# Performance work log

Hardware: AMD Instinct MI355X
Metric: run time of the kernel (lower is better)

The kernel has to match this reference:

```python
import jax, jax.numpy as jnp
import numpy as np

N, E, IN, HID, G, OUT = 50000, 800000, 9, 128, 256, 10
CLUSTERS, NCO, MCO = 20, 6, 4  # numerator deg 5 (6 coeffs), denominator deg 4
EPS = 1e-5


def _gcn(x, W, b, src, dst):
    # PyG GCNConv: x' = D^-1/2 (A + I) D^-1/2 (x W) + b, with self-loops
    n = x.shape[0]
    h = x @ W  # [N, out]
    ones = jnp.ones(src.shape[0], h.dtype)
    deg = jax.ops.segment_sum(ones, dst, num_segments=n) + 1.0  # + self-loop
    dinv = jax.lax.rsqrt(deg)
    coef = (dinv[src] * dinv[dst])[:, None]
    agg = jax.ops.segment_sum(h[src] * coef, dst, num_segments=n)
    agg = agg + h * (dinv * dinv)[:, None]  # self-loop messages
    return agg + b


def _rational(x, num, den, assign):
    # per-cluster safe Pade rational: P_5(x) / (1 + |Q_4(x)|), coeffs gathered per channel
    a = num[assign]  # [HID, 6]
    q = den[assign]  # [HID, 4]
    P = a[:, 5]
    for i in (4, 3, 2, 1, 0):
        P = P * x + a[:, i]
    Q = q[:, 3]
    for i in (2, 1, 0):
        Q = Q * x + q[:, i]
    Q = Q * x  # Q has no constant term
    return P / (1.0 + jnp.abs(Q))


def _bn(x, g, b):
    m = x.mean(axis=0)
    v = x.var(axis=0)
    return g * (x - m) * jax.lax.rsqrt(v + EPS) + b


def setup_inputs() -> dict:
    key = jax.random.key(0)
    ks = jax.random.split(key, 32)
    d = {}
    d["x"] = jax.random.normal(ks[0], (N, IN), jnp.float32)
    d["edge_index"] = jax.random.randint(ks[1], (2, E), 0, N, jnp.int32)
    d["batch"] = jnp.sort(jax.random.randint(ks[2], (N,), 0, G, jnp.int32))
    dims = [(IN, HID), (HID, HID), (HID, HID), (HID, HID)]
    for i, (di, do) in enumerate(dims):
        d[f"W{i}"] = jax.random.normal(ks[3 + i], (di, do), jnp.float32) / np.sqrt(di)
        d[f"b{i}"] = jnp.zeros((do,), jnp.float32)
        d[f"g{i}"] = jnp.ones((do,), jnp.float32)
        d[f"be{i}"] = jnp.zeros((do,), jnp.float32)
    d["rat_num"] = jax.random.normal(ks[10], (CLUSTERS, NCO), jnp.float32) * 0.3
    d["rat_den"] = jax.random.normal(ks[11], (CLUSTERS, MCO), jnp.float32) * 0.3
    d["cluster_assign"] = (jnp.arange(HID) % CLUSTERS).astype(jnp.int32)
    d["HW1"] = jax.random.normal(ks[12], (HID, HID), jnp.float32) / np.sqrt(HID)
    d["Hb1"] = jnp.zeros((HID,), jnp.float32)
    d["HW2"] = jax.random.normal(ks[13], (HID, HID), jnp.float32) / np.sqrt(HID)
    d["Hb2"] = jnp.zeros((HID,), jnp.float32)
    d["HW3"] = jax.random.normal(ks[14], (HID, OUT), jnp.float32) / np.sqrt(HID)
    d["Hb3"] = jnp.zeros((OUT,), jnp.float32)
    return d


def reference(x, edge_index, batch,
              W0, b0, g0, be0, W1, b1, g1, be1,
              W2, b2, g2, be2, W3, b3, g3, be3,
              rat_num, rat_den, cluster_assign,
              HW1, Hb1, HW2, Hb2, HW3, Hb3):
    src, dst = edge_index[0], edge_index[1]
    h = x
    for W, b, g, be in ((W0, b0, g0, be0), (W1, b1, g1, be1),
                        (W2, b2, g2, be2), (W3, b3, g3, be3)):
        h = _gcn(h, W, b, src, dst)
        h = _rational(h, rat_num, rat_den, cluster_assign)
        h = _bn(h, g, be)
        # Dropout(p=0.1): identity in eval mode
    # global mean pool over graphs
    counts = jax.ops.segment_sum(jnp.ones((h.shape[0],), h.dtype), batch, num_segments=G)
    pooled = jax.ops.segment_sum(h, batch, num_segments=G) / jnp.maximum(counts, 1.0)[:, None]
    # MLP head: (Dropout->Linear->GELU) x2, Dropout->Linear
    z = jax.nn.gelu(pooled @ HW1 + Hb1, approximate=False)
    z = jax.nn.gelu(z @ HW2 + Hb2, approximate=False)
    return z @ HW3 + Hb3
```

## Files before the change

kernel.cpp:

```cpp
#include <hip/hip_runtime.h>
#include <math.h>

#define HID 128
#define GRP 256
#define INF 9
#define OUTF 10

typedef _Float16 half8 __attribute__((ext_vector_type(8)));
typedef __attribute__((ext_vector_type(4))) float f32x4;

__global__ void hist_prepw_kernel(const int* __restrict__ ei, int* __restrict__ cnt, int E,
                                  const float* __restrict__ W1, const float* __restrict__ W2,
                                  const float* __restrict__ W3,
                                  _Float16* __restrict__ Whi, _Float16* __restrict__ Wlo) {
    int e = blockIdx.x * 256 + threadIdx.x;
    if (e < E) atomicAdd(&cnt[ei[E + e]], 1);
    if (blockIdx.x < 192) {
        int l = blockIdx.x >> 6;
        int idx = (blockIdx.x & 63) * 256 + threadIdx.x;
        const float* W = (l == 0) ? W1 : (l == 1) ? W2 : W3;
        int nn = idx >> 7, k = idx & 127;
        float w = W[k * HID + nn];
        _Float16 hi = (_Float16)w;
        _Float16 lo = (_Float16)(w - (float)hi);
        int nt = nn >> 4, l16 = nn & 15;
        int kc = k >> 5, quad = (k >> 3) & 3, j = k & 7;
        size_t off = (size_t)(l + 1) * HID * HID +
                     ((((nt * 4 + kc) * 4 + quad) * 16 + l16) * 8 + j);
        Whi[off] = hi;
        Wlo[off] = lo;
    }
}

__global__ __launch_bounds__(256) void scanA_kernel(const int* __restrict__ cnt,
                                                    int* __restrict__ bsum, int n) {
    int tid = threadIdx.x;
    int base = blockIdx.x * 1024 + tid * 4;
    int s = 0;
    #pragma unroll
    for (int i = 0; i < 4; i++) s += (base + i < n) ? cnt[base + i] : 0;
    #pragma unroll
    for (int off = 32; off > 0; off >>= 1) s += __shfl_down(s, off);
    __shared__ int ws[4];
    if ((tid & 63) == 0) ws[tid >> 6] = s;
    __syncthreads();
    if (tid == 0) bsum[blockIdx.x] = ws[0] + ws[1] + ws[2] + ws[3];
}

__global__ void scanB_kernel(int* __restrict__ bsum, int* __restrict__ row_ptr,
                             int nb, int n) {
    int lane = threadIdx.x;
    int carry = 0;
    for (int base = 0; base < nb; base += 64) {
        int v = (base + lane < nb) ? bsum[base + lane] : 0;
        int ps = v;
        #pragma unroll
        for (int off = 1; off < 64; off <<= 1) {
            int t = __shfl_up(ps, off);
            if (lane >= off) ps += t;
        }
        if (base + lane < nb) bsum[base + lane] = carry + ps - v;
        carry += __shfl(ps, 63);
    }
    if (lane == 0) row_ptr[n] = carry;
}

__global__ __launch_bounds__(256) void scanC_kernel(const int* __restrict__ cnt,
                                                    const int* __restrict__ bsum,
                                                    const int* __restrict__ batch,
                                                    int* __restrict__ row_ptr,
                                                    int* __restrict__ cursor,
                                                    float* __restrict__ dinv,
                                                    int* __restrict__ gstart,
                                                    int* __restrict__ gend, int n) {
    int tid = threadIdx.x;
    int lane = tid & 63, wid = tid >> 6;
    int idx0 = blockIdx.x * 1024 + tid * 4;
    int v[4];
    #pragma unroll
    for (int i = 0; i < 4; i++) v[i] = (idx0 + i < n) ? cnt[idx0 + i] : 0;
    int s = v[0] + v[1] + v[2] + v[3];
    int ps = s;
    #pragma unroll
    for (int off = 1; off < 64; off <<= 1) {
        int t = __shfl_up(ps, off);
        if (lane >= off) ps += t;
    }
    __shared__ int wsum[4];
    if (lane == 63) wsum[wid] = ps;
    __syncthreads();
    int woff = 0;
    #pragma unroll
    for (int i = 0; i < 4; i++) if (i < wid) woff += wsum[i];
    int run = bsum[blockIdx.x] + woff + (ps - s);
    #pragma unroll
    for (int i = 0; i < 4; i++) {
        int idx = idx0 + i;
        if (idx < n) {
            row_ptr[idx] = run;
            cursor[idx] = run;
            dinv[idx] = rsqrtf((float)(v[i] + 1));
            run += v[i];
            int b = batch[idx];
            if (idx == 0 || batch[idx - 1] != b) gstart[b] = idx;
            if (idx == n - 1 || batch[idx + 1] != b) gend[b] = idx + 1;
        }
    }
}

__global__ void fill_kernel(const int* __restrict__ ei, int* __restrict__ cursor,
                            const float* __restrict__ dinv,
                            int2* __restrict__ csr, int E) {
    int e = blockIdx.x * blockDim.x + threadIdx.x;
    if (e >= E) return;
    int s = ei[e], d = ei[E + e];
    int pos = atomicAdd(&cursor[d], 1);
    csr[pos] = make_int2(s, __float_as_int(dinv[s] * dinv[d]));
}

__device__ __forceinline__ float rational_act(float xv, const float* __restrict__ a,
                                              const float* __restrict__ q) {
    float P = a[5];
    P = fmaf(P, xv, a[4]); P = fmaf(P, xv, a[3]); P = fmaf(P, xv, a[2]);
    P = fmaf(P, xv, a[1]); P = fmaf(P, xv, a[0]);
    float Q = q[3];
    Q = fmaf(Q, xv, q[2]); Q = fmaf(Q, xv, q[1]); Q = fmaf(Q, xv, q[0]);
    Q *= xv;
    return P / (1.0f + fabsf(Q));
}

__global__ __launch_bounds__(256) void aggx_kernel(const float* __restrict__ x,
                                                   const int* __restrict__ row_ptr,
                                                   const int2* __restrict__ csr,
                                                   const float* __restrict__ dinv,
                                                   float* __restrict__ aggX,
                                                   float* __restrict__ cagg, int n) {
    int tid = threadIdx.x;
    int node = blockIdx.x * 16 + (tid >> 4);
    int lane = tid & 15;
    if (node >= n) return;
    float di = dinv[node];
    float self = di * di;
    float acc = (lane < INF) ? x[node * INF + lane] * self : 0.0f;
    float cfs = self;
    int beg = row_ptr[node], end = row_ptr[node + 1];
    for (int j = beg; j < end; j++) {
        int2 p = csr[j];
        float cf = __int_as_float(p.y);
        cfs += cf;
        if (lane < INF) acc = fmaf(cf, x[p.x * INF + lane], acc);
    }
    if (lane < INF) aggX[node * INF + lane] = acc;
    if (lane == 0) cagg[node] = cfs;
}

__global__ __launch_bounds__(256) void gemm0_fused_kernel(const float* __restrict__ aggX,
                                                          const float* __restrict__ W0,
                                                          const float* __restrict__ b0,
                                                          const float* __restrict__ rat_num,
                                                          const float* __restrict__ rat_den,
                                                          const int* __restrict__ cl_assign,
                                                          _Float16* __restrict__ act,
                                                          float* __restrict__ stat, int n) {
    __shared__ float Ws[INF * HID];
    __shared__ float s_num[120], s_den[80];
    __shared__ int s_cl[HID];
    __shared__ float s_b[HID];
    __shared__ float s_sum[HID], s_sq[HID];
    int tid = threadIdx.x;
    for (int i = tid; i < INF * HID; i += 256) Ws[i] = W0[i];
    if (tid < 120) s_num[tid] = rat_num[tid];
    if (tid < 80) s_den[tid] = rat_den[tid];
    if (tid < HID) {
        s_cl[tid] = cl_assign[tid];
        s_b[tid] = b0[tid];
        s_sum[tid] = 0.0f; s_sq[tid] = 0.0f;
    }
    __syncthreads();
    int c = tid & 127;
    int half = tid >> 7;
    const float* a = s_num + s_cl[c] * 6;
    const float* q = s_den + s_cl[c] * 4;
    float psum = 0.0f, psq = 0.0f;
    for (int node = blockIdx.x * 2 + half; node < n; node += gridDim.x * 2) {
        float acc = s_b[c];
        #pragma unroll
        for (int k = 0; k < INF; k++) acc = fmaf(aggX[node * INF + k], Ws[k * HID + c], acc);
        float r = rational_act(acc, a, q);
        act[node * HID + c] = (_Float16)r;
        psum += r; psq = fmaf(r, r, psq);
    }
    atomicAdd(&s_sum[c], psum);
    atomicAdd(&s_sq[c], psq);
    __syncthreads();
    if (tid < HID) {
        atomicAdd(&stat[tid], s_sum[tid]);
        atomicAdd(&stat[HID + tid], s_sq[tid]);
    }
}

__global__ __launch_bounds__(256) void layer_fused_kernel(const _Float16* __restrict__ act,
                                                          const int2* __restrict__ csr,
                                                          const int* __restrict__ row_ptr,
                                                          const float* __restrict__ dinv,
                                                          const float* __restrict__ cagg,
                                                          const float* __restrict__ statPrev,
                                                          const float* __restrict__ gPrev,
                                                          const float* __restrict__ bePrev,
                                                          const _Float16* __restrict__ Whi,
                                                          const _Float16* __restrict__ Wlo,
                                                          const float* __restrict__ bias,
                                                          const float* __restrict__ rat_num,
                                                          const float* __restrict__ rat_den,
                                                          const int* __restrict__ cl_assign,
                                                          _Float16* __restrict__ actOut,
                                                          float* __restrict__ statOut, int n) {
    __shared__ _Float16 Alds[64 * 136];
    __shared__ int2 s_pair[16][16];
    __shared__ float s_bnw[HID], s_bnu[HID];
    __shared__ float s_num[120], s_den[80];
    __shared__ int s_cl[HID];
    __shared__ float s_bias[HID];
    __shared__ float s_sum[HID], s_sq[HID];
    int tid = threadIdx.x;
    if (tid < 120) s_num[tid] = rat_num[tid];
    if (tid < 80) s_den[tid] = rat_den[tid];
    if (tid < HID) {
        float inv_n = 1.0f / (float)n;
        float mean = statPrev[tid] * inv_n;
        float var = statPrev[HID + tid] * inv_n - mean * mean;
        float w = gPrev[tid] * rsqrtf(var + 1e-5f);
        s_bnw[tid] = w;
        s_bnu[tid] = bePrev[tid] - mean * w;
        s_cl[tid] = cl_assign[tid];
        s_bias[tid] = bias[tid];
        s_sum[tid] = 0.0f; s_sq[tid] = 0.0f;
    }
    __syncthreads();

    int r0 = blockIdx.x * 64;
    int grp = tid >> 4, glane = tid & 15;
    const half8* act8 = (const half8*)act;

    for (int sub = 0; sub < 4; sub++) {
        int lrow = sub * 16 + grp;
        int node = r0 + lrow;
        half8 o;
        if (node < n) {
            float di = dinv[node];
            float selfc = di * di;
            half8 sv = act8[node * 16 + glane];
            float acc[8];
            #pragma unroll
            for (int t = 0; t < 8; t++) acc[t] = (float)sv[t] * selfc;
            int beg = row_ptr[node], end = row_ptr[node + 1];
            for (int base = beg; base < end; base += 16) {
                int m = end - base; if (m > 16) m = 16;
                if (glane < m) s_pair[grp][glane] = csr[base + glane];
                __builtin_amdgcn_wave_barrier();
                int j = 0;
                for (; j + 4 <= m; j += 4) {
                    int2 p0 = s_pair[grp][j],     p1 = s_pair[grp][j + 1];
                    int2 p2 = s_pair[grp][j + 2], p3 = s_pair[grp][j + 3];
                    half8 v0 = act8[p0.x * 16 + glane];
                    half8 v1 = act8[p1.x * 16 + glane];
                    half8 v2 = act8[p2.x * 16 + glane];
                    half8 v3 = act8[p3.x * 16 + glane];
                    float c0 = __int_as_float(p0.y), c1 = __int_as_float(p1.y);
                    float c2 = __int_as_float(p2.y), c3 = __int_as_float(p3.y);
                    #pragma unroll
                    for (int t = 0; t < 8; t++) {
                        acc[t] = fmaf(c0, (float)v0[t], acc[t]);
                        acc[t] = fmaf(c1, (float)v1[t], acc[t]);
                        acc[t] = fmaf(c2, (float)v2[t], acc[t]);
                        acc[t] = fmaf(c3, (float)v3[t], acc[t]);
                    }
                }
                for (; j < m; j++) {
                    int2 p = s_pair[grp][j];
                    float cf = __int_as_float(p.y);
                    half8 v = act8[p.x * 16 + glane];
                    #pragma unroll
                    for (int t = 0; t < 8; t++) acc[t] = fmaf(cf, (float)v[t], acc[t]);
                }
                __builtin_amdgcn_wave_barrier();
            }
            float cg = cagg[node];
            #pragma unroll
            for (int t = 0; t < 8; t++) {
                int c = glane * 8 + t;
                o[t] = (_Float16)fmaf(s_bnw[c], acc[t], s_bnu[c] * cg);
            }
        } else {
            #pragma unroll
            for (int t = 0; t < 8; t++) o[t] = (_Float16)0.0f;
        }
        *(half8*)&Alds[lrow * 136 + glane * 8] = o;
    }
    __syncthreads();

    int w = tid >> 6, l64 = tid & 63;
    int quad = l64 >> 4, l16 = l64 & 15;
    const half8* Bh8 = (const half8*)Whi;
    const half8* Bl8 = (const half8*)Wlo;
    f32x4 acc[8];
    #pragma unroll
    for (int j = 0; j < 8; j++) acc[j] = (f32x4){0.f, 0.f, 0.f, 0.f};
    int lrowA = w * 16 + l16;
    #pragma unroll
    for (int kc = 0; kc < 4; kc++) {
        half8 a = *(const half8*)&Alds[lrowA * 136 + kc * 32 + quad * 8];
        #pragma unroll
        for (int nt = 0; nt < 8; nt++) {
            half8 bh = Bh8[(nt * 4 + kc) * 64 + l64];
            half8 bl = Bl8[(nt * 4 + kc) * 64 + l64];
            acc[nt] = __builtin_amdgcn_mfma_f32_16x16x32_f16(a, bh, acc[nt], 0, 0, 0);
            acc[nt] = __builtin_amdgcn_mfma_f32_16x16x32_f16(a, bl, acc[nt], 0, 0, 0);
        }
    }

    float ps[8], pq[8];
    #pragma unroll
    for (int nt = 0; nt < 8; nt++) { ps[nt] = 0.0f; pq[nt] = 0.0f; }
    #pragma unroll
    for (int reg = 0; reg < 4; reg++) {
        int row = r0 + w * 16 + quad * 4 + reg;
        if (row < n) {
            #pragma unroll
            for (int nt = 0; nt < 8; nt++) {
                int col = nt * 16 + l16;
                float v = acc[nt][reg] + s_bias[col];
                float r = rational_act(v, s_num + s_cl[col] * 6, s_den + s_cl[col] * 4);
                actOut[row * HID + col] = (_Float16)r;
                ps[nt] += r; pq[nt] = fmaf(r, r, pq[nt]);
            }
        }
    }
    #pragma unroll
    for (int nt = 0; nt < 8; nt++) {
        int col = nt * 16 + l16;
        atomicAdd(&s_sum[col], ps[nt]);
        atomicAdd(&s_sq[col], pq[nt]);
    }
    __syncthreads();
    if (tid < HID) {
        atomicAdd(&statOut[tid], s_sum[tid]);
        atomicAdd(&statOut[HID + tid], s_sq[tid]);
    }
}

__global__ __launch_bounds__(256) void poolmlp_kernel(const _Float16* __restrict__ act,
                                                      const int* __restrict__ gstart,
                                                      const int* __restrict__ gend,
                                                      const float* __restrict__ stat,
                                                      const float* __restrict__ g3,
                                                      const float* __restrict__ be3,
                                                      const float* __restrict__ HW1,
                                                      const float* __restrict__ Hb1,
                                                      const float* __restrict__ HW2,
                                                      const float* __restrict__ Hb2,
                                                      const float* __restrict__ HW3,
                                                      const float* __restrict__ Hb3,
                                                      float* __restrict__ out, int n) {
    __shared__ float red[16][HID];
    __shared__ float s_pool[HID];
    __shared__ float s_z[HID];
    int gi = blockIdx.x;
    int tid = threadIdx.x;
    int rg = tid >> 4, lane = tid & 15;
    int s = gstart[gi], e = gend[gi];
    const half8* act8 = (const half8*)act;
    float a[8];
    #pragma unroll
    for (int t = 0; t < 8; t++) a[t] = 0.0f;
    for (int r = s + rg; r < e; r += 16) {
        half8 v = act8[r * 16 + lane];
        #pragma unroll
        for (int t = 0; t < 8; t++) a[t] += (float)v[t];
    }
    #pragma unroll
    for (int t = 0; t < 8; t++) red[rg][lane * 8 + t] = a[t];
    __syncthreads();
    if (tid < HID) {
        float tot = 0.0f;
        #pragma unroll
        for (int i = 0; i < 16; i++) tot += red[i][tid];
        int cnt = e - s;
        float pooled = 0.0f;
        if (cnt > 0) {
            float inv_n = 1.0f / (float)n;
            float mean = stat[tid] * inv_n;
            float var = stat[HID + tid] * inv_n - mean * mean;
            float w = g3[tid] * rsqrtf(var + 1e-5f);
            float u = be3[tid] - mean * w;
            pooled = fmaf(w, tot / (float)cnt, u);
        }
        s_pool[tid] = pooled;
    }
    __syncthreads();
    if (tid < HID) {
        float acc = Hb1[tid];
        #pragma unroll 8
        for (int k = 0; k < HID; k++) acc = fmaf(s_pool[k], HW1[k * HID + tid], acc);
        s_z[tid] = 0.5f * acc * (1.0f + erff(acc * 0.70710678118654752f));
    }
    __syncthreads();
    if (tid < HID) {
        float acc = Hb2[tid];
        #pragma unroll 8
        for (int k = 0; k < HID; k++) acc = fmaf(s_z[k], HW2[k * HID + tid], acc);
        s_pool[tid] = 0.5f * acc * (1.0f + erff(acc * 0.70710678118654752f));
    }
    __syncthreads();
    if (tid < OUTF) {
        float acc = Hb3[tid];
        #pragma unroll 8
        for (int k = 0; k < HID; k++) acc = fmaf(s_pool[k], HW3[k * OUTF + tid], acc);
        out[gi * OUTF + tid] = acc;
    }
}

extern "C" void kernel_launch(void* const* d_in, const int* in_sizes, int n_in,
                              void* d_out, int out_size, void* d_ws, size_t ws_size,
                              hipStream_t stream) {
    const float* x          = (const float*)d_in[0];
    const int*   edge_index = (const int*)d_in[1];
    const int*   batch      = (const int*)d_in[2];
    const float* W[4]  = {(const float*)d_in[3], (const float*)d_in[7], (const float*)d_in[11], (const float*)d_in[15]};
    const float* bL[4] = {(const float*)d_in[4], (const float*)d_in[8], (const float*)d_in[12], (const float*)d_in[16]};
    const float* gL[4] = {(const float*)d_in[5], (const float*)d_in[9], (const float*)d_in[13], (const float*)d_in[17]};
    const float* beL[4]= {(const float*)d_in[6], (const float*)d_in[10], (const float*)d_in[14], (const float*)d_in[18]};
    const float* rat_num = (const float*)d_in[19];
    const float* rat_den = (const float*)d_in[20];
    const int*   cl_assign = (const int*)d_in[21];
    const float* HW1 = (const float*)d_in[22];
    const float* Hb1 = (const float*)d_in[23];
    const float* HW2 = (const float*)d_in[24];
    const float* Hb2 = (const float*)d_in[25];
    const float* HW3 = (const float*)d_in[26];
    const float* Hb3 = (const float*)d_in[27];
    float* out = (float*)d_out;

    const int N = in_sizes[0] / INF;
    const int E = in_sizes[1] / 2;
    const int NB = (N + 1023) / 1024;

    char* wsb = (char*)d_ws;
    size_t o = 0;
    #define ALIGN16 o = (o + 3) & ~(size_t)3;
    int*   cnt     = (int*)(wsb + o * 4);  o += N; ALIGN16
    int*   gstart  = (int*)(wsb + o * 4);  o += GRP;
    int*   gend    = (int*)(wsb + o * 4);  o += GRP;
    float* bnstat  = (float*)(wsb + o * 4); o += 4 * 256;
    size_t zero_elems = o;
    int*   bsum    = (int*)(wsb + o * 4);  o += ((NB + 63) & ~63); ALIGN16
    int*   cursor  = (int*)(wsb + o * 4);  o += N; ALIGN16
    int*   row_ptr = (int*)(wsb + o * 4);  o += N + 1; ALIGN16
    float* dinv    = (float*)(wsb + o * 4); o += N; ALIGN16
    int2*  csr     = (int2*)(wsb + o * 4);  o += 2 * (size_t)E; ALIGN16
    float* aggX    = (float*)(wsb + o * 4); o += (size_t)N * INF; ALIGN16
    _Float16* WhiAll = (_Float16*)(wsb + o * 4); o += 4 * HID * HID / 2; ALIGN16
    _Float16* WloAll = (_Float16*)(wsb + o * 4); o += 4 * HID * HID / 2; ALIGN16
    _Float16* act_h  = (_Float16*)(wsb + o * 4); o += (size_t)N * HID / 2;
    float* cagg = (float*)cnt;

    hipMemsetAsync(d_ws, 0, zero_elems * 4, stream);

    int eb = (E + 255) / 256;
    hist_prepw_kernel<<<eb, 256, 0, stream>>>(edge_index, cnt, E, W[1], W[2], W[3],
                                              WhiAll, WloAll);
    scanA_kernel<<<NB, 256, 0, stream>>>(cnt, bsum, N);
    scanB_kernel<<<1, 64, 0, stream>>>(bsum, row_ptr, NB, N);
    scanC_kernel<<<NB, 256, 0, stream>>>(cnt, bsum, batch, row_ptr, cursor, dinv,
                                         gstart, gend, N);
    fill_kernel<<<eb, 256, 0, stream>>>(edge_index, cursor, dinv, csr, E);

    aggx_kernel<<<(N + 15) / 16, 256, 0, stream>>>(x, row_ptr, csr, dinv, aggX, cagg, N);
    gemm0_fused_kernel<<<1024, 256, 0, stream>>>(aggX, W[0], bL[0], rat_num, rat_den,
                                                 cl_assign, act_h, bnstat, N);

    int layer_grid = (N + 63) / 64;
    for (int l = 1; l < 4; l++) {
        layer_fused_kernel<<<layer_grid, 256, 0, stream>>>(act_h, csr, row_ptr, dinv, cagg,
                                                           bnstat + (l - 1) * 256,
                                                           gL[l - 1], beL[l - 1],
                                                           WhiAll + (size_t)l * HID * HID,
                                                           WloAll + (size_t)l * HID * HID,
                                                           bL[l], rat_num, rat_den, cl_assign,
                                                           act_h, bnstat + l * 256, N);
    }
    poolmlp_kernel<<<GRP, 256, 0, stream>>>(act_h, gstart, gend, bnstat + 3 * 256,
                                            gL[3], beL[3], HW1, Hb1, HW2, Hb2, HW3, Hb3,
                                            out, N);
}
```

Before: 516.1 us.

## Use 512-thread 32-row blocks with wave-split MFMA and ping-pong activations

The fused GCN layer kernel now launches 512-thread blocks covering 32 nodes. Each 16-lane group aggregates a single node instead of looping over four, and the 128x128 MFMA GEMM is split across 8 waves as 2 row tiles by 4 column pairs. This is meant to expose more parallelism for the latency-bound neighbour gather and to cut per-thread accumulator registers. Activations also move from one buffer updated in place to two alternating buffers. That removes a read-after-write race between blocks gathering neighbour rows, at the cost of an extra N×128 half buffer.

```diff
diff --git a/kernel.cpp b/kernel.cpp
--- a/kernel.cpp
+++ b/kernel.cpp
@@ -199,7 +199,7 @@
     }
 }
 
-__global__ __launch_bounds__(256) void layer_fused_kernel(const _Float16* __restrict__ act,
+__global__ __launch_bounds__(512, 8) void layer_fused_kernel(const _Float16* __restrict__ act,
                                                           const int2* __restrict__ csr,
                                                           const int* __restrict__ row_ptr,
                                                           const float* __restrict__ dinv,
@@ -215,8 +215,8 @@
                                                           const int* __restrict__ cl_assign,
                                                           _Float16* __restrict__ actOut,
                                                           float* __restrict__ statOut, int n) {
-    __shared__ _Float16 Alds[64 * 136];
-    __shared__ int2 s_pair[16][16];
+    __shared__ _Float16 Alds[32 * 136];
+    __shared__ int2 s_pair[32][16];
     __shared__ float s_bnw[HID], s_bnu[HID];
     __shared__ float s_num[120], s_den[80];
     __shared__ int s_cl[HID];
@@ -238,13 +238,12 @@
     }
     __syncthreads();
 
-    int r0 = blockIdx.x * 64;
+    int r0 = blockIdx.x * 32;
     int grp = tid >> 4, glane = tid & 15;
     const half8* act8 = (const half8*)act;
 
-    for (int sub = 0; sub < 4; sub++) {
-        int lrow = sub * 16 + grp;
-        int node = r0 + lrow;
+    {
+        int node = r0 + grp;
         half8 o;
         if (node < n) {
             float di = dinv[node];
@@ -295,53 +294,53 @@
             #pragma unroll
             for (int t = 0; t < 8; t++) o[t] = (_Float16)0.0f;
         }
-        *(half8*)&Alds[lrow * 136 + glane * 8] = o;
+        *(half8*)&Alds[grp * 136 + glane * 8] = o;
     }
     __syncthreads();
 
     int w = tid >> 6, l64 = tid & 63;
     int quad = l64 >> 4, l16 = l64 & 15;
+    int mtile = w & 1, npair = w >> 1;
     const half8* Bh8 = (const half8*)Whi;
     const half8* Bl8 = (const half8*)Wlo;
-    f32x4 acc[8];
-    #pragma unroll
-    for (int j = 0; j < 8; j++) acc[j] = (f32x4){0.f, 0.f, 0.f, 0.f};
-    int lrowA = w * 16 + l16;
+    f32x4 acc0 = (f32x4){0.f, 0.f, 0.f, 0.f};
+    f32x4 acc1 = (f32x4){0.f, 0.f, 0.f, 0.f};
+    int lrowA = mtile * 16 + l16;
     #pragma unroll
     for (int kc = 0; kc < 4; kc++) {
         half8 a = *(const half8*)&Alds[lrowA * 136 + kc * 32 + quad * 8];
-        #pragma unroll
-        for (int nt = 0; nt < 8; nt++) {
-            half8 bh = Bh8[(nt * 4 + kc) * 64 + l64];
-            half8 bl = Bl8[(nt * 4 + kc) * 64 + l64];
-            acc[nt] = __builtin_amdgcn_mfma_f32_16x16x32_f16(a, bh, acc[nt], 0, 0, 0);
-            acc[nt] = __builtin_amdgcn_mfma_f32_16x16x32_f16(a, bl, acc[nt], 0, 0, 0);
+        int nt0 = npair * 2, nt1 = npair * 2 + 1;
+        half8 bh0 = Bh8[(nt0 * 4 + kc) * 64 + l64];
+        half8 bl0 = Bl8[(nt0 * 4 + kc) * 64 + l64];
+        half8 bh1 = Bh8[(nt1 * 4 + kc) * 64 + l64];
+        half8 bl1 = Bl8[(nt1 * 4 + kc) * 64 + l64];
+        acc0 = __builtin_amdgcn_mfma_f32_16x16x32_f16(a, bh0, acc0, 0, 0, 0);
+        acc0 = __builtin_amdgcn_mfma_f32_16x16x32_f16(a, bl0, acc0, 0, 0, 0);
+        acc1 = __builtin_amdgcn_mfma_f32_16x16x32_f16(a, bh1, acc1, 0, 0, 0);
+        acc1 = __builtin_amdgcn_mfma_f32_16x16x32_f16(a, bl1, acc1, 0, 0, 0);
+    }
+
+    float ps0 = 0.f, pq0 = 0.f, ps1 = 0.f, pq1 = 0.f;
+    int col0 = (npair * 2) * 16 + l16;
+    int col1 = (npair * 2 + 1) * 16 + l16;
+    #pragma unroll
+    for (int reg = 0; reg < 4; reg++) {
+        int row = r0 + mtile * 16 + quad * 4 + reg;
+        if (row < n) {
+            float v0 = acc0[reg] + s_bias[col0];
+            float r0v = rational_act(v0, s_num + s_cl[col0] * 6, s_den + s_cl[col0] * 4);
+            actOut[row * HID + col0] = (_Float16)r0v;
+            ps0 += r0v; pq0 = fmaf(r0v, r0v, pq0);
+            float v1 = acc1[reg] + s_bias[col1];
+            float r1v = rational_act(v1, s_num + s_cl[col1] * 6, s_den + s_cl[col1] * 4);
+            actOut[row * HID + col1] = (_Float16)r1v;
+            ps1 += r1v; pq1 = fmaf(r1v, r1v, pq1);
         }
     }
-
-    float ps[8], pq[8];
-    #pragma unroll
-    for (int nt = 0; nt < 8; nt++) { ps[nt] = 0.0f; pq[nt] = 0.0f; }
-    #pragma unroll
-    for (int reg = 0; reg < 4; reg++) {
-        int row = r0 + w * 16 + quad * 4 + reg;
-        if (row < n) {
-            #pragma unroll
-            for (int nt = 0; nt < 8; nt++) {
-                int col = nt * 16 + l16;
-                float v = acc[nt][reg] + s_bias[col];
-                float r = rational_act(v, s_num + s_cl[col] * 6, s_den + s_cl[col] * 4);
-                actOut[row * HID + col] = (_Float16)r;
-                ps[nt] += r; pq[nt] = fmaf(r, r, pq[nt]);
-            }
-        }
-    }
-    #pragma unroll
-    for (int nt = 0; nt < 8; nt++) {
-        int col = nt * 16 + l16;
-        atomicAdd(&s_sum[col], ps[nt]);
-        atomicAdd(&s_sq[col], pq[nt]);
-    }
+    atomicAdd(&s_sum[col0], ps0);
+    atomicAdd(&s_sq[col0], pq0);
+    atomicAdd(&s_sum[col1], ps1);
+    atomicAdd(&s_sq[col1], pq1);
     __syncthreads();
     if (tid < HID) {
         atomicAdd(&statOut[tid], s_sum[tid]);
@@ -461,7 +460,8 @@
     float* aggX    = (float*)(wsb + o * 4); o += (size_t)N * INF; ALIGN16
     _Float16* WhiAll = (_Float16*)(wsb + o * 4); o += 4 * HID * HID / 2; ALIGN16
     _Float16* WloAll = (_Float16*)(wsb + o * 4); o += 4 * HID * HID / 2; ALIGN16
-    _Float16* act_h  = (_Float16*)(wsb + o * 4); o += (size_t)N * HID / 2;
+    _Float16* actA   = (_Float16*)(wsb + o * 4); o += (size_t)N * HID / 2; ALIGN16
+    _Float16* actB   = (_Float16*)(wsb + o * 4); o += (size_t)N * HID / 2;
     float* cagg = (float*)cnt;
 
     hipMemsetAsync(d_ws, 0, zero_elems * 4, stream);
@@ -477,19 +477,22 @@
 
     aggx_kernel<<<(N + 15) / 16, 256, 0, stream>>>(x, row_ptr, csr, dinv, aggX, cagg, N);
     gemm0_fused_kernel<<<1024, 256, 0, stream>>>(aggX, W[0], bL[0], rat_num, rat_den,
-                                                 cl_assign, act_h, bnstat, N);
-
-    int layer_grid = (N + 63) / 64;
+                                                 cl_assign, actA, bnstat, N);
+
+    _Float16* bufs[2] = {actA, actB};
+    int layer_grid = (N + 31) / 32;
     for (int l = 1; l < 4; l++) {
-        layer_fused_kernel<<<layer_grid, 256, 0, stream>>>(act_h, csr, row_ptr, dinv, cagg,
+        _Float16* src = bufs[(l - 1) & 1];
+        _Float16* dst = bufs[l & 1];
+        layer_fused_kernel<<<layer_grid, 512, 0, stream>>>(src, csr, row_ptr, dinv, cagg,
                                                            bnstat + (l - 1) * 256,
                                                            gL[l - 1], beL[l - 1],
                                                            WhiAll + (size_t)l * HID * HID,
                                                            WloAll + (size_t)l * HID * HID,
                                                            bL[l], rat_num, rat_den, cl_assign,
-                                                           act_h, bnstat + l * 256, N);
-    }
-    poolmlp_kernel<<<GRP, 256, 0, stream>>>(act_h, gstart, gend, bnstat + 3 * 256,
+                                                           dst, bnstat + l * 256, N);
+    }
+    poolmlp_kernel<<<GRP, 256, 0, stream>>>(bufs[3 & 1], gstart, gend, bnstat + 3 * 256,
                                             gL[3], beL[3], HW1, Hb1, HW2, Hb2, HW3, Hb3,
                                             out, N);
 }
```

After: 568.8 us. 10.2% more time.

## Split fused GCN layer into separate aggregation and MFMA GEMM kernels

Applied to the files above, without the earlier changes.

Each hidden layer is no longer one kernel that aggregates 64 nodes into LDS and then runs the MFMA GEMM. It is now two kernels: a neighbour-aggregation kernel that handles 16 nodes per block and writes the BN-normalized aggregate to a new global fp16 buffer, and a GEMM+rational+stats kernel that reads that buffer. The gather loop is also unrolled to 8 neighbours to keep more loads in flight. The aim is finer-grained scheduling, better load balance and higher occupancy for the irregular gather, which no longer waits behind the GEMM phase. The cost is an extra write and read of an N×128 fp16 intermediate and one more launch per layer. It also removes the in-place read/write hazard on the activation buffer.

```diff
diff --git a/kernel.cpp b/kernel.cpp
--- a/kernel.cpp
+++ b/kernel.cpp
@@ -199,32 +199,18 @@
     }
 }
 
-__global__ __launch_bounds__(256) void layer_fused_kernel(const _Float16* __restrict__ act,
-                                                          const int2* __restrict__ csr,
-                                                          const int* __restrict__ row_ptr,
-                                                          const float* __restrict__ dinv,
-                                                          const float* __restrict__ cagg,
-                                                          const float* __restrict__ statPrev,
-                                                          const float* __restrict__ gPrev,
-                                                          const float* __restrict__ bePrev,
-                                                          const _Float16* __restrict__ Whi,
-                                                          const _Float16* __restrict__ Wlo,
-                                                          const float* __restrict__ bias,
-                                                          const float* __restrict__ rat_num,
-                                                          const float* __restrict__ rat_den,
-                                                          const int* __restrict__ cl_assign,
-                                                          _Float16* __restrict__ actOut,
-                                                          float* __restrict__ statOut, int n) {
-    __shared__ _Float16 Alds[64 * 136];
+__global__ __launch_bounds__(256) void agg_kernel(const _Float16* __restrict__ act,
+                                                  const int* __restrict__ row_ptr,
+                                                  const int2* __restrict__ csr,
+                                                  const float* __restrict__ dinv,
+                                                  const float* __restrict__ cagg,
+                                                  const float* __restrict__ statPrev,
+                                                  const float* __restrict__ gPrev,
+                                                  const float* __restrict__ bePrev,
+                                                  _Float16* __restrict__ A, int n) {
+    __shared__ float s_bnw[HID], s_bnu[HID];
     __shared__ int2 s_pair[16][16];
-    __shared__ float s_bnw[HID], s_bnu[HID];
-    __shared__ float s_num[120], s_den[80];
-    __shared__ int s_cl[HID];
-    __shared__ float s_bias[HID];
-    __shared__ float s_sum[HID], s_sq[HID];
-    int tid = threadIdx.x;
-    if (tid < 120) s_num[tid] = rat_num[tid];
-    if (tid < 80) s_den[tid] = rat_den[tid];
+    int tid = threadIdx.x;
     if (tid < HID) {
         float inv_n = 1.0f / (float)n;
         float mean = statPrev[tid] * inv_n;
@@ -232,88 +218,133 @@
         float w = gPrev[tid] * rsqrtf(var + 1e-5f);
         s_bnw[tid] = w;
         s_bnu[tid] = bePrev[tid] - mean * w;
+    }
+    __syncthreads();
+    int row = tid >> 4, lane = tid & 15;
+    int node = blockIdx.x * 16 + row;
+    if (node >= n) return;
+    const half8* act8 = (const half8*)act;
+    float di = dinv[node];
+    float selfc = di * di;
+    half8 sv = act8[node * 16 + lane];
+    float acc[8];
+    #pragma unroll
+    for (int t = 0; t < 8; t++) acc[t] = (float)sv[t] * selfc;
+    int beg = row_ptr[node], end = row_ptr[node + 1];
+    for (int base = beg; base < end; base += 16) {
+        int m = end - base; if (m > 16) m = 16;
+        if (lane < m) s_pair[row][lane] = csr[base + lane];
+        __builtin_amdgcn_wave_barrier();
+        int j = 0;
+        for (; j + 8 <= m; j += 8) {
+            int2 p0 = s_pair[row][j],     p1 = s_pair[row][j + 1];
+            int2 p2 = s_pair[row][j + 2], p3 = s_pair[row][j + 3];
+            int2 p4 = s_pair[row][j + 4], p5 = s_pair[row][j + 5];
+            int2 p6 = s_pair[row][j + 6], p7 = s_pair[row][j + 7];
+            half8 v0 = act8[p0.x * 16 + lane];
+            half8 v1 = act8[p1.x * 16 + lane];
+            half8 v2 = act8[p2.x * 16 + lane];
+            half8 v3 = act8[p3.x * 16 + lane];
+            half8 v4 = act8[p4.x * 16 + lane];
+            half8 v5 = act8[p5.x * 16 + lane];
+            half8 v6 = act8[p6.x * 16 + lane];
+            half8 v7 = act8[p7.x * 16 + lane];
+            float c0 = __int_as_float(p0.y), c1 = __int_as_float(p1.y);
+            float c2 = __int_as_float(p2.y), c3 = __int_as_float(p3.y);
+            float c4 = __int_as_float(p4.y), c5 = __int_as_float(p5.y);
+            float c6 = __int_as_float(p6.y), c7 = __int_as_float(p7.y);
+            #pragma unroll
+            for (int t = 0; t < 8; t++) {
+                acc[t] = fmaf(c0, (float)v0[t], acc[t]);
+                acc[t] = fmaf(c1, (float)v1[t], acc[t]);
+                acc[t] = fmaf(c2, (float)v2[t], acc[t]);
+                acc[t] = fmaf(c3, (float)v3[t], acc[t]);
+                acc[t] = fmaf(c4, (float)v4[t], acc[t]);
+                acc[t] = fmaf(c5, (float)v5[t], acc[t]);
+                acc[t] = fmaf(c6, (float)v6[t], acc[t]);
+                acc[t] = fmaf(c7, (float)v7[t], acc[t]);
+            }
+        }
+        for (; j + 4 <= m; j += 4) {
+            int2 p0 = s_pair[row][j],     p1 = s_pair[row][j + 1];
+            int2 p2 = s_pair[row][j + 2], p3 = s_pair[row][j + 3];
+            half8 v0 = act8[p0.x * 16 + lane];
+            half8 v1 = act8[p1.x * 16 + lane];
+            half8 v2 = act8[p2.x * 16 + lane];
+            half8 v3 = act8[p3.x * 16 + lane];
+            float c0 = __int_as_float(p0.y), c1 = __int_as_float(p1.y);
+            float c2 = __int_as_float(p2.y), c3 = __int_as_float(p3.y);
+            #pragma unroll
+            for (int t = 0; t < 8; t++) {
+                acc[t] = fmaf(c0, (float)v0[t], acc[t]);
+                acc[t] = fmaf(c1, (float)v1[t], acc[t]);
+                acc[t] = fmaf(c2, (float)v2[t], acc[t]);
+                acc[t] = fmaf(c3, (float)v3[t], acc[t]);
+            }
+        }
+        for (; j < m; j++) {
+            int2 p = s_pair[row][j];
+            float cf = __int_as_float(p.y);
+            half8 v = act8[p.x * 16 + lane];
+            #pragma unroll
+            for (int t = 0; t < 8; t++) acc[t] = fmaf(cf, (float)v[t], acc[t]);
+        }
+        __builtin_amdgcn_wave_barrier();
+    }
+    float cg = cagg[node];
+    half8 o;
+    #pragma unroll
+    for (int t = 0; t < 8; t++) {
+        int c = lane * 8 + t;
+        o[t] = (_Float16)fmaf(s_bnw[c], acc[t], s_bnu[c] * cg);
+    }
+    ((half8*)A)[node * 16 + lane] = o;
+}
+
+__global__ __launch_bounds__(256) void gemm_mfma_kernel(const _Float16* __restrict__ A,
+                                                        const _Float16* __restrict__ Whi,
+                                                        const _Float16* __restrict__ Wlo,
+                                                        const float* __restrict__ bias,
+                                                        const float* __restrict__ rat_num,
+                                                        const float* __restrict__ rat_den,
+                                                        const int* __restrict__ cl_assign,
+                                                        _Float16* __restrict__ act,
+                                                        float* __restrict__ stat, int n) {
+    __shared__ float s_num[120], s_den[80];
+    __shared__ int s_cl[HID];
+    __shared__ float s_bias[HID];
+    __shared__ float s_sum[HID], s_sq[HID];
+    int tid = threadIdx.x;
+    if (tid < 120) s_num[tid] = rat_num[tid];
+    if (tid < 80) s_den[tid] = rat_den[tid];
+    if (tid < HID) {
         s_cl[tid] = cl_assign[tid];
         s_bias[tid] = bias[tid];
         s_sum[tid] = 0.0f; s_sq[tid] = 0.0f;
     }
     __syncthreads();
 
-    int r0 = blockIdx.x * 64;
-    int grp = tid >> 4, glane = tid & 15;
-    const half8* act8 = (const half8*)act;
-
-    for (int sub = 0; sub < 4; sub++) {
-        int lrow = sub * 16 + grp;
-        int node = r0 + lrow;
-        half8 o;
-        if (node < n) {
-            float di = dinv[node];
-            float selfc = di * di;
-            half8 sv = act8[node * 16 + glane];
-            float acc[8];
-            #pragma unroll
-            for (int t = 0; t < 8; t++) acc[t] = (float)sv[t] * selfc;
-            int beg = row_ptr[node], end = row_ptr[node + 1];
-            for (int base = beg; base < end; base += 16) {
-                int m = end - base; if (m > 16) m = 16;
-                if (glane < m) s_pair[grp][glane] = csr[base + glane];
-                __builtin_amdgcn_wave_barrier();
-                int j = 0;
-                for (; j + 4 <= m; j += 4) {
-                    int2 p0 = s_pair[grp][j],     p1 = s_pair[grp][j + 1];
-                    int2 p2 = s_pair[grp][j + 2], p3 = s_pair[grp][j + 3];
-                    half8 v0 = act8[p0.x * 16 + glane];
-                    half8 v1 = act8[p1.x * 16 + glane];
-                    half8 v2 = act8[p2.x * 16 + glane];
-                    half8 v3 = act8[p3.x * 16 + glane];
-                    float c0 = __int_as_float(p0.y), c1 = __int_as_float(p1.y);
-                    float c2 = __int_as_float(p2.y), c3 = __int_as_float(p3.y);
-                    #pragma unroll
-                    for (int t = 0; t < 8; t++) {
-                        acc[t] = fmaf(c0, (float)v0[t], acc[t]);
-                        acc[t] = fmaf(c1, (float)v1[t], acc[t]);
-                        acc[t] = fmaf(c2, (float)v2[t], acc[t]);
-                        acc[t] = fmaf(c3, (float)v3[t], acc[t]);
-                    }
-                }
-                for (; j < m; j++) {
-                    int2 p = s_pair[grp][j];
-                    float cf = __int_as_float(p.y);
-                    half8 v = act8[p.x * 16 + glane];
-                    #pragma unroll
-                    for (int t = 0; t < 8; t++) acc[t] = fmaf(cf, (float)v[t], acc[t]);
-                }
-                __builtin_amdgcn_wave_barrier();
-            }
-            float cg = cagg[node];
-            #pragma unroll
-            for (int t = 0; t < 8; t++) {
-                int c = glane * 8 + t;
-                o[t] = (_Float16)fmaf(s_bnw[c], acc[t], s_bnu[c] * cg);
-            }
-        } else {
-            #pragma unroll
-            for (int t = 0; t < 8; t++) o[t] = (_Float16)0.0f;
-        }
-        *(half8*)&Alds[lrow * 136 + glane * 8] = o;
-    }
-    __syncthreads();
-
-    int w = tid >> 6, l64 = tid & 63;
-    int quad = l64 >> 4, l16 = l64 & 15;
+    int w = tid >> 6, lane = tid & 63;
+    int quad = lane >> 4, l16 = lane & 15;
+    int r0 = blockIdx.x * 64 + w * 16;
+
+    const half8* A8 = (const half8*)A;
     const half8* Bh8 = (const half8*)Whi;
     const half8* Bl8 = (const half8*)Wlo;
+
     f32x4 acc[8];
     #pragma unroll
     for (int j = 0; j < 8; j++) acc[j] = (f32x4){0.f, 0.f, 0.f, 0.f};
-    int lrowA = w * 16 + l16;
+
+    int rowA = r0 + l16;
+    int rcA = (rowA < n) ? rowA : 0;
     #pragma unroll
     for (int kc = 0; kc < 4; kc++) {
-        half8 a = *(const half8*)&Alds[lrowA * 136 + kc * 32 + quad * 8];
+        half8 a = A8[rcA * 16 + kc * 4 + quad];
         #pragma unroll
         for (int nt = 0; nt < 8; nt++) {
-            half8 bh = Bh8[(nt * 4 + kc) * 64 + l64];
-            half8 bl = Bl8[(nt * 4 + kc) * 64 + l64];
+            half8 bh = Bh8[(nt * 4 + kc) * 64 + lane];
+            half8 bl = Bl8[(nt * 4 + kc) * 64 + lane];
             acc[nt] = __builtin_amdgcn_mfma_f32_16x16x32_f16(a, bh, acc[nt], 0, 0, 0);
             acc[nt] = __builtin_amdgcn_mfma_f32_16x16x32_f16(a, bl, acc[nt], 0, 0, 0);
         }
@@ -324,14 +355,14 @@
     for (int nt = 0; nt < 8; nt++) { ps[nt] = 0.0f; pq[nt] = 0.0f; }
     #pragma unroll
     for (int reg = 0; reg < 4; reg++) {
-        int row = r0 + w * 16 + quad * 4 + reg;
+        int row = r0 + quad * 4 + reg;
         if (row < n) {
             #pragma unroll
             for (int nt = 0; nt < 8; nt++) {
                 int col = nt * 16 + l16;
                 float v = acc[nt][reg] + s_bias[col];
                 float r = rational_act(v, s_num + s_cl[col] * 6, s_den + s_cl[col] * 4);
-                actOut[row * HID + col] = (_Float16)r;
+                act[row * HID + col] = (_Float16)r;
                 ps[nt] += r; pq[nt] = fmaf(r, r, pq[nt]);
             }
         }
@@ -344,8 +375,8 @@
     }
     __syncthreads();
     if (tid < HID) {
-        atomicAdd(&statOut[tid], s_sum[tid]);
-        atomicAdd(&statOut[HID + tid], s_sq[tid]);
+        atomicAdd(&stat[tid], s_sum[tid]);
+        atomicAdd(&stat[HID + tid], s_sq[tid]);
     }
 }
 
@@ -461,7 +492,8 @@
     float* aggX    = (float*)(wsb + o * 4); o += (size_t)N * INF; ALIGN16
     _Float16* WhiAll = (_Float16*)(wsb + o * 4); o += 4 * HID * HID / 2; ALIGN16
     _Float16* WloAll = (_Float16*)(wsb + o * 4); o += 4 * HID * HID / 2; ALIGN16
-    _Float16* act_h  = (_Float16*)(wsb + o * 4); o += (size_t)N * HID / 2;
+    _Float16* act_h  = (_Float16*)(wsb + o * 4); o += (size_t)N * HID / 2; ALIGN16
+    _Float16* A_h    = (_Float16*)(wsb + o * 4); o += (size_t)N * HID / 2;
     float* cagg = (float*)cnt;
 
     hipMemsetAsync(d_ws, 0, zero_elems * 4, stream);
@@ -479,15 +511,17 @@
     gemm0_fused_kernel<<<1024, 256, 0, stream>>>(aggX, W[0], bL[0], rat_num, rat_den,
                                                  cl_assign, act_h, bnstat, N);
 
-    int layer_grid = (N + 63) / 64;
+    int agg_grid = (N + 15) / 16;
+    int gemm_grid = (N + 63) / 64;
     for (int l = 1; l < 4; l++) {
-        layer_fused_kernel<<<layer_grid, 256, 0, stream>>>(act_h, csr, row_ptr, dinv, cagg,
-                                                           bnstat + (l - 1) * 256,
-                                                           gL[l - 1], beL[l - 1],
-                                                           WhiAll + (size_t)l * HID * HID,
-                                                           WloAll + (size_t)l * HID * HID,
-                                                           bL[l], rat_num, rat_den, cl_assign,
-                                                           act_h, bnstat + l * 256, N);
+        agg_kernel<<<agg_grid, 256, 0, stream>>>(act_h, row_ptr, csr, dinv, cagg,
+                                                 bnstat + (l - 1) * 256,
+                                                 gL[l - 1], beL[l - 1], A_h, N);
+        gemm_mfma_kernel<<<gemm_grid, 256, 0, stream>>>(A_h,
+                                                        WhiAll + (size_t)l * HID * HID,
+                                                        WloAll + (size_t)l * HID * HID, bL[l],
+                                                        rat_num, rat_den, cl_assign,
+                                                        act_h, bnstat + l * 256, N);
     }
     poolmlp_kernel<<<GRP, 256, 0, stream>>>(act_h, gstart, gend, bnstat + 3 * 256,
                                             gL[3], beL[3], HW1, Hb1, HW2, Hb2, HW3, Hb3,
```

Result: slower. 544.3 us (+5.5%).
